# Kernel tuning notes

Measured on AMD Instinct MI355X. Metric: run time of the kernel, lower is better.

Reference implementation:

```python
import jax, jax.numpy as jnp
import numpy as np

B, S, IN, OUT, GS = 4, 2048, 4096, 16384, 32
G = IN // GS  # 128 groups per row


def setup_inputs() -> dict:
    key = jax.random.key(0)
    kx, ks, ki = jax.random.split(key, 3)
    x = jax.random.normal(kx, (B, S, IN), dtype=jnp.float32)
    # n_bits=2 initial codebook from the module
    codebook = jnp.array([-1.0, -0.25, 0.25, 1.0], dtype=jnp.float32)
    # scale is the log of per-group max-abs (use_exp_for_scale=True)
    scale = jax.random.normal(ks, (OUT, G, 1), dtype=jnp.float32) * 0.1 - 2.0
    indexes = jax.random.randint(ki, (OUT, G, GS), 0, 4, dtype=jnp.int32)
    return {"x": x, "codebook": codebook, "scale": scale, "indexes": indexes}


def reference(x, codebook, scale, indexes):
    # dequantize_weight: normalize codebook, gather per-element, exp-scale per group
    cb_norm = codebook / jnp.clip(jnp.max(jnp.abs(codebook)), 1e-8, None)
    w = cb_norm[indexes] * jnp.exp(scale)          # (OUT, G, GS)
    w = w.reshape(OUT, IN)                         # (OUT, IN)
    # F.linear(x, w) = x @ w.T
    return jnp.einsum("bsi,oi->bso", x, w)
```

## Files before the change

### kernel.cpp

```cpp
#include <hip/hip_runtime.h>
#include <stdint.h>


typedef unsigned short u16;
typedef __attribute__((ext_vector_type(8))) __bf16 bf16x8;
typedef __attribute__((ext_vector_type(4))) float f32x4;

__device__ __forceinline__ uint32_t f2bf(float f) {
  uint32_t u = __builtin_bit_cast(uint32_t, f);
  return (u + 0x7FFFu + ((u >> 16) & 1u)) >> 16;
}

__device__ __forceinline__ void gload16(const u16* g, u16* l) {
  __builtin_amdgcn_global_load_lds(
      (__attribute__((address_space(1))) void*)(g),
      (__attribute__((address_space(3))) void*)(l), 16, 0, 0);
}

__device__ __forceinline__ uint32_t sel4(uint32_t b0, uint32_t b1, uint32_t b2,
                                         uint32_t b3, int q) {
  uint32_t lo = (q & 1) ? b1 : b0;
  uint32_t hi = (q & 1) ? b3 : b2;
  return (q & 2) ? hi : lo;
}

__global__ __launch_bounds__(256) void cvt_x(const float* __restrict__ x,
                                             u16* __restrict__ xb, int n8) {
  int t = blockIdx.x * 256 + threadIdx.x;
  if (t >= n8) return;
  const float4* xp = reinterpret_cast<const float4*>(x) + (size_t)t * 2;
  float4 v0 = xp[0], v1 = xp[1];
  uint4 o;
  o.x = f2bf(v0.x) | (f2bf(v0.y) << 16);
  o.y = f2bf(v0.z) | (f2bf(v0.w) << 16);
  o.z = f2bf(v1.x) | (f2bf(v1.y) << 16);
  o.w = f2bf(v1.z) | (f2bf(v1.w) << 16);
  reinterpret_cast<uint4*>(xb)[t] = o;
}

__global__ __launch_bounds__(256) void dequant_w(
    const float* __restrict__ cb, const float* __restrict__ scale,
    const int* __restrict__ idx, u16* __restrict__ w, int ngroups) {
  int t = blockIdx.x * 256 + threadIdx.x;
  if (t >= ngroups) return;
  float m = fmaxf(fmaxf(fabsf(cb[0]), fabsf(cb[1])),
                  fmaxf(fabsf(cb[2]), fabsf(cb[3])));
  m = fmaxf(m, 1e-8f);
  float s = expf(scale[t]) / m;
  uint32_t b0 = f2bf(cb[0] * s), b1 = f2bf(cb[1] * s);
  uint32_t b2 = f2bf(cb[2] * s), b3 = f2bf(cb[3] * s);
  const int4* ip = reinterpret_cast<const int4*>(idx) + (size_t)t * 8;
  uint4* op = reinterpret_cast<uint4*>(w) + (size_t)t * 4;
#pragma unroll
  for (int v = 0; v < 4; ++v) {
    int4 qa = ip[v * 2], qb = ip[v * 2 + 1];
    uint4 o;
    o.x = sel4(b0, b1, b2, b3, qa.x) | (sel4(b0, b1, b2, b3, qa.y) << 16);
    o.y = sel4(b0, b1, b2, b3, qa.z) | (sel4(b0, b1, b2, b3, qa.w) << 16);
    o.z = sel4(b0, b1, b2, b3, qb.x) | (sel4(b0, b1, b2, b3, qb.y) << 16);
    o.w = sel4(b0, b1, b2, b3, qb.z) | (sel4(b0, b1, b2, b3, qb.w) << 16);
    op[v] = o;
  }
}

#define BM 256
#define BN 256
#define BK 64

__device__ __forceinline__ void memfence() { asm volatile("" ::: "memory"); }
__device__ __forceinline__ void BARx() {
  memfence();
  __builtin_amdgcn_s_barrier();
  memfence();
}

__global__ void __launch_bounds__(512, 2) gemm256(
    const u16* __restrict__ A, const u16* __restrict__ Bt,
    float* __restrict__ C, int M, int N, int K) {
  __shared__ u16 sm[2][2][BM * BK];

  const int nwg = gridDim.x;
  const int cpx = nwg >> 3;
  const int bid = blockIdx.x;
  const int swz = (bid & 7) * cpx + (bid >> 3);
  const int ntn = N / BN;
  const int m0 = (swz / ntn) * BM;
  const int n0 = (swz % ntn) * BN;

  const int tid = threadIdx.x;
  const int lane = tid & 63;
  const int wid = tid >> 6;
  const int wr = wid >> 2;
  const int wc = wid & 3;

  const int srow = wid * 8 + (lane >> 3);
  const int scol = (((lane & 7) ^ ((lane >> 3) & 7)) << 3);
  const u16* gA = A + (size_t)(m0 + srow) * K + scol;
  const u16* gB = Bt + (size_t)(n0 + srow) * K + scol;

#define STAGE(b, op, h, gp, kc)                                   \
  {                                                               \
    u16* d = &sm[(b)][(op)][(h)*8192 + wid * 512];                \
    const u16* g = (gp) + (size_t)((h)*128) * K + (kc);           \
    gload16(g, d);                                                \
    gload16(g + (size_t)64 * K, d + 4096);                        \
  }

  const int swzp0 = (((lane >> 4) ^ (lane & 7)) << 3);
  const int swzp1 = ((((lane >> 4) + 4) ^ (lane & 7)) << 3);
  const int lr = lane & 15;
  const int rAbase = (wr * 64 + lr) * BK;
  const int rBbase = (wc * 32 + lr) * BK;

  bf16x8 af[4][2], bv[2][2];

#define LOADA(b, q)                                               \
  {                                                               \
    const u16* p = &sm[(b)][0][rAbase + (q)*8192];                \
    af[0][0] = *(const bf16x8*)(p + swzp0);                       \
    af[0][1] = *(const bf16x8*)(p + swzp1);                       \
    af[1][0] = *(const bf16x8*)(p + 1024 + swzp0);                \
    af[1][1] = *(const bf16x8*)(p + 1024 + swzp1);                \
    af[2][0] = *(const bf16x8*)(p + 2048 + swzp0);                \
    af[2][1] = *(const bf16x8*)(p + 2048 + swzp1);                \
    af[3][0] = *(const bf16x8*)(p + 3072 + swzp0);                \
    af[3][1] = *(const bf16x8*)(p + 3072 + swzp1);                \
  }
#define LOADB(b, pp)                                              \
  {                                                               \
    const u16* p = &sm[(b)][1][rBbase + (pp)*8192];               \
    bv[0][0] = *(const bf16x8*)(p + swzp0);                       \
    bv[0][1] = *(const bf16x8*)(p + swzp1);                       \
    bv[1][0] = *(const bf16x8*)(p + 1024 + swzp0);                \
    bv[1][1] = *(const bf16x8*)(p + 1024 + swzp1);                \
  }
#define MFMAQ(q, pp)                                                        \
  {                                                                         \
    __builtin_amdgcn_s_setprio(1);                                          \
    _Pragma("unroll") for (int i = 0; i < 4; ++i)                           \
        _Pragma("unroll") for (int j = 0; j < 2; ++j)                       \
            _Pragma("unroll") for (int ks = 0; ks < 2; ++ks)                \
                acc[(q)*4 + i][(pp)*2 + j] =                                \
        __builtin_amdgcn_mfma_f32_16x16x32_bf16(                            \
            af[i][ks], bv[j][ks], acc[(q)*4 + i][(pp)*2 + j], 0, 0, 0);     \
    __builtin_amdgcn_s_setprio(0);                                          \
  }
#define VM6 asm volatile("s_waitcnt vmcnt(6)" ::: "memory");
#define VM0 asm volatile("s_waitcnt vmcnt(0)" ::: "memory");

  f32x4 acc[8][4];
#pragma unroll
  for (int i = 0; i < 8; ++i)
#pragma unroll
    for (int j = 0; j < 4; ++j) acc[i][j] = f32x4{0.f, 0.f, 0.f, 0.f};

  STAGE(0, 0, 0, gA, (size_t)0)
  STAGE(0, 1, 1, gB, (size_t)0)
  STAGE(0, 0, 1, gA, (size_t)0)
  STAGE(0, 1, 0, gB, (size_t)0)
  STAGE(1, 0, 0, gA, (size_t)64)
  STAGE(1, 1, 1, gB, (size_t)64)
  STAGE(1, 0, 1, gA, (size_t)64)
  VM6
  BARx();

#pragma unroll 1
  for (int i = 0; i < 31; ++i) {
    const size_t cS1 = (size_t)(2 * i + 1) * 64;
    const size_t cb0 = (size_t)(2 * i + 2) * 64;
    const size_t cb1 = (size_t)(2 * i + 3) * 64;
    LOADA(0, 0) LOADB(0, 0)
    STAGE(1, 1, 0, gB, cS1)
    BARx(); MFMAQ(0, 0) BARx();
    LOADB(0, 1)
    STAGE(0, 0, 0, gA, cb0)
    BARx(); MFMAQ(0, 1) BARx();
    LOADA(0, 1)
    STAGE(0, 1, 1, gB, cb0)
    BARx(); MFMAQ(1, 1) BARx();
    LOADB(0, 0)
    STAGE(0, 0, 1, gA, cb0)
    BARx(); MFMAQ(1, 0) VM6 BARx();
    LOADA(1, 0) LOADB(1, 0)
    STAGE(0, 1, 0, gB, cb0)
    BARx(); MFMAQ(0, 0) BARx();
    LOADB(1, 1)
    STAGE(1, 0, 0, gA, cb1)
    BARx(); MFMAQ(0, 1) BARx();
    LOADA(1, 1)
    STAGE(1, 1, 1, gB, cb1)
    BARx(); MFMAQ(1, 1) BARx();
    LOADB(1, 0)
    STAGE(1, 0, 1, gA, cb1)
    BARx(); MFMAQ(1, 0) VM6 BARx();
  }

  {
    const size_t cS1 = (size_t)63 * 64;
    LOADA(0, 0) LOADB(0, 0)
    STAGE(1, 1, 0, gB, cS1)
    BARx(); MFMAQ(0, 0) BARx();
    LOADB(0, 1)
    BARx(); MFMAQ(0, 1) BARx();
    LOADA(0, 1)
    BARx(); MFMAQ(1, 1) BARx();
    LOADB(0, 0)
    BARx(); MFMAQ(1, 0) VM0 BARx();
    LOADA(1, 0) LOADB(1, 0)
    BARx(); MFMAQ(0, 0) BARx();
    LOADB(1, 1)
    BARx(); MFMAQ(0, 1) BARx();
    LOADA(1, 1)
    BARx(); MFMAQ(1, 1) BARx();
    LOADB(1, 0)
    BARx(); MFMAQ(1, 0)
  }

  const int crow0 = m0 + wr * 64 + ((lane >> 4) << 2);
  const int ccol0 = n0 + wc * 32 + (lane & 15);
#pragma unroll
  for (int q = 0; q < 2; ++q)
#pragma unroll
    for (int mi = 0; mi < 4; ++mi)
#pragma unroll
      for (int r = 0; r < 4; ++r) {
        float* cp = C + (size_t)(crow0 + q * 128 + mi * 16 + r) * N + ccol0;
#pragma unroll
        for (int pp = 0; pp < 2; ++pp)
#pragma unroll
          for (int j = 0; j < 2; ++j)
            cp[pp * 128 + j * 16] = acc[q * 4 + mi][pp * 2 + j][r];
      }
}

extern "C" void kernel_launch(void* const* d_in, const int* in_sizes, int n_in,
                              void* d_out, int out_size, void* d_ws,
                              size_t ws_size, hipStream_t stream) {
  const float* x = (const float*)d_in[0];
  const float* cb = (const float*)d_in[1];
  const float* scale = (const float*)d_in[2];
  const int* idx = (const int*)d_in[3];
  float* out = (float*)d_out;

  constexpr int M = 4 * 2048;
  constexpr int N = 16384;
  constexpr int K = 4096;

  u16* xb = (u16*)d_ws;
  u16* wb = xb + (size_t)M * K;

  const int n8 = M * K / 8;
  cvt_x<<<dim3(n8 / 256), dim3(256), 0, stream>>>(x, xb, n8);
  const int ngroups = N * (K / 32);
  dequant_w<<<dim3(ngroups / 256), dim3(256), 0, stream>>>(cb, scale, idx, wb,
                                                           ngroups);
  gemm256<<<dim3((M / BM) * (N / BN)), dim3(512), 0, stream>>>(xb, wb, out, M,
                                                               N, K);
}
```

Baseline: 1.054 ms.

## Switch GEMM inner loop to 32x32x16 MFMA with batched LDS reads

Replaces the 16x16x32 bf16 MFMA tiling with 32x32x16 MFMAs, which changes the per-wave fragment layout, the LDS swizzled read offsets and the output store mapping. All A and B fragments for a K-half are now read from LDS once per buffer instead of being interleaved between MFMA quarters. The goal is fewer LDS reads per MFMA and higher MFMA throughput. In exchange the kernel holds more fragment registers at once, which may raise register pressure at 2 blocks per CU, and the LDS reads are no longer overlapped with the MFMA phases.

```diff
diff --git a/kernel.cpp b/kernel.cpp
--- a/kernel.cpp
+++ b/kernel.cpp
@@ -4,7 +4,7 @@
 
 typedef unsigned short u16;
 typedef __attribute__((ext_vector_type(8))) __bf16 bf16x8;
-typedef __attribute__((ext_vector_type(4))) float f32x4;
+typedef __attribute__((ext_vector_type(16))) float f32x16;
 
 __device__ __forceinline__ uint32_t f2bf(float f) {
   uint32_t u = __builtin_bit_cast(uint32_t, f);
@@ -90,8 +90,9 @@
   const int tid = threadIdx.x;
   const int lane = tid & 63;
   const int wid = tid >> 6;
-  const int wr = wid >> 2;
-  const int wc = wid & 3;
+  const int wr = wid >> 1;
+  const int wrm = wid >> 2;
+  const int wcn = wid & 3;
 
   const int srow = wid * 8 + (lane >> 3);
   const int scol = (((lane & 7) ^ ((lane >> 3) & 7)) << 3);
@@ -106,53 +107,53 @@
     gload16(g + (size_t)64 * K, d + 4096);                        \
   }
 
-  const int swzp0 = (((lane >> 4) ^ (lane & 7)) << 3);
-  const int swzp1 = ((((lane >> 4) + 4) ^ (lane & 7)) << 3);
-  const int lr = lane & 15;
-  const int rAbase = (wr * 64 + lr) * BK;
-  const int rBbase = (wc * 32 + lr) * BK;
-
-  bf16x8 af[4][2], bv[2][2];
-
-#define LOADA(b, q)                                               \
-  {                                                               \
-    const u16* p = &sm[(b)][0][rAbase + (q)*8192];                \
-    af[0][0] = *(const bf16x8*)(p + swzp0);                       \
-    af[0][1] = *(const bf16x8*)(p + swzp1);                       \
-    af[1][0] = *(const bf16x8*)(p + 1024 + swzp0);                \
-    af[1][1] = *(const bf16x8*)(p + 1024 + swzp1);                \
-    af[2][0] = *(const bf16x8*)(p + 2048 + swzp0);                \
-    af[2][1] = *(const bf16x8*)(p + 2048 + swzp1);                \
-    af[3][0] = *(const bf16x8*)(p + 3072 + swzp0);                \
-    af[3][1] = *(const bf16x8*)(p + 3072 + swzp1);                \
-  }
-#define LOADB(b, pp)                                              \
-  {                                                               \
-    const u16* p = &sm[(b)][1][rBbase + (pp)*8192];               \
-    bv[0][0] = *(const bf16x8*)(p + swzp0);                       \
-    bv[0][1] = *(const bf16x8*)(p + swzp1);                       \
-    bv[1][0] = *(const bf16x8*)(p + 1024 + swzp0);                \
-    bv[1][1] = *(const bf16x8*)(p + 1024 + swzp1);                \
-  }
-#define MFMAQ(q, pp)                                                        \
-  {                                                                         \
-    __builtin_amdgcn_s_setprio(1);                                          \
-    _Pragma("unroll") for (int i = 0; i < 4; ++i)                           \
-        _Pragma("unroll") for (int j = 0; j < 2; ++j)                       \
-            _Pragma("unroll") for (int ks = 0; ks < 2; ++ks)                \
-                acc[(q)*4 + i][(pp)*2 + j] =                                \
-        __builtin_amdgcn_mfma_f32_16x16x32_bf16(                            \
-            af[i][ks], bv[j][ks], acc[(q)*4 + i][(pp)*2 + j], 0, 0, 0);     \
-    __builtin_amdgcn_s_setprio(0);                                          \
+  const int l7 = lane & 7;
+  const int hi5 = lane >> 5;
+  const int l31 = lane & 31;
+  int sw[4];
+#pragma unroll
+  for (int ks = 0; ks < 4; ++ks) sw[ks] = (((ks * 2 + hi5) ^ l7) << 3);
+  const int rAoff = (wrm * 64 + l31) * BK;
+  const int rBoff = (wcn * 32 + l31) * BK;
+
+  bf16x8 a0[2][4], a1[2][4], bv[2][4];
+
+#define ALLREADS(b)                                                     \
+  {                                                                     \
+    const u16* pa = &sm[(b)][0][rAoff];                                 \
+    const u16* pb = &sm[(b)][1][rBoff];                                 \
+    _Pragma("unroll") for (int mi = 0; mi < 2; ++mi)                    \
+        _Pragma("unroll") for (int ks = 0; ks < 4; ++ks)                \
+            a0[mi][ks] = *(const bf16x8*)(pa + mi * 2048 + sw[ks]);     \
+    _Pragma("unroll") for (int ks = 0; ks < 4; ++ks)                    \
+        bv[0][ks] = *(const bf16x8*)(pb + sw[ks]);                      \
+    _Pragma("unroll") for (int ks = 0; ks < 4; ++ks)                    \
+        bv[1][ks] = *(const bf16x8*)(pb + 8192 + sw[ks]);               \
+    _Pragma("unroll") for (int mi = 0; mi < 2; ++mi)                    \
+        _Pragma("unroll") for (int ks = 0; ks < 4; ++ks)                \
+            a1[mi][ks] = *(const bf16x8*)(pa + 8192 + mi * 2048 + sw[ks]); \
+  }
+
+#define MFMAQ(q, pp, AF)                                                \
+  {                                                                     \
+    __builtin_amdgcn_s_setprio(1);                                      \
+    _Pragma("unroll") for (int mi = 0; mi < 2; ++mi)                    \
+        _Pragma("unroll") for (int ks = 0; ks < 4; ++ks)                \
+            acc[(q)*2 + mi][(pp)] =                                     \
+        __builtin_amdgcn_mfma_f32_32x32x16_bf16(                        \
+            AF[mi][ks], bv[(pp)][ks], acc[(q)*2 + mi][(pp)], 0, 0, 0);  \
+    __builtin_amdgcn_s_setprio(0);                                      \
   }
 #define VM6 asm volatile("s_waitcnt vmcnt(6)" ::: "memory");
 #define VM0 asm volatile("s_waitcnt vmcnt(0)" ::: "memory");
 
-  f32x4 acc[8][4];
-#pragma unroll
-  for (int i = 0; i < 8; ++i)
-#pragma unroll
-    for (int j = 0; j < 4; ++j) acc[i][j] = f32x4{0.f, 0.f, 0.f, 0.f};
+  f32x16 acc[4][2];
+#pragma unroll
+  for (int i = 0; i < 4; ++i)
+#pragma unroll
+    for (int j = 0; j < 2; ++j)
+#pragma unroll
+      for (int r = 0; r < 16; ++r) acc[i][j][r] = 0.f;
 
   STAGE(0, 0, 0, gA, (size_t)0)
   STAGE(0, 1, 1, gB, (size_t)0)
@@ -169,67 +170,53 @@
     const size_t cS1 = (size_t)(2 * i + 1) * 64;
     const size_t cb0 = (size_t)(2 * i + 2) * 64;
     const size_t cb1 = (size_t)(2 * i + 3) * 64;
-    LOADA(0, 0) LOADB(0, 0)
+    ALLREADS(0)
     STAGE(1, 1, 0, gB, cS1)
-    BARx(); MFMAQ(0, 0) BARx();
-    LOADB(0, 1)
+    BARx(); MFMAQ(0, 0, a0) BARx();
     STAGE(0, 0, 0, gA, cb0)
-    BARx(); MFMAQ(0, 1) BARx();
-    LOADA(0, 1)
+    BARx(); MFMAQ(0, 1, a0) BARx();
     STAGE(0, 1, 1, gB, cb0)
-    BARx(); MFMAQ(1, 1) BARx();
-    LOADB(0, 0)
+    BARx(); MFMAQ(1, 1, a1) BARx();
     STAGE(0, 0, 1, gA, cb0)
-    BARx(); MFMAQ(1, 0) VM6 BARx();
-    LOADA(1, 0) LOADB(1, 0)
+    BARx(); MFMAQ(1, 0, a1) VM6 BARx();
+    ALLREADS(1)
     STAGE(0, 1, 0, gB, cb0)
-    BARx(); MFMAQ(0, 0) BARx();
-    LOADB(1, 1)
+    BARx(); MFMAQ(0, 0, a0) BARx();
     STAGE(1, 0, 0, gA, cb1)
-    BARx(); MFMAQ(0, 1) BARx();
-    LOADA(1, 1)
+    BARx(); MFMAQ(0, 1, a0) BARx();
     STAGE(1, 1, 1, gB, cb1)
-    BARx(); MFMAQ(1, 1) BARx();
-    LOADB(1, 0)
+    BARx(); MFMAQ(1, 1, a1) BARx();
     STAGE(1, 0, 1, gA, cb1)
-    BARx(); MFMAQ(1, 0) VM6 BARx();
+    BARx(); MFMAQ(1, 0, a1) VM6 BARx();
   }
 
   {
     const size_t cS1 = (size_t)63 * 64;
-    LOADA(0, 0) LOADB(0, 0)
+    ALLREADS(0)
     STAGE(1, 1, 0, gB, cS1)
-    BARx(); MFMAQ(0, 0) BARx();
-    LOADB(0, 1)
-    BARx(); MFMAQ(0, 1) BARx();
-    LOADA(0, 1)
-    BARx(); MFMAQ(1, 1) BARx();
-    LOADB(0, 0)
-    BARx(); MFMAQ(1, 0) VM0 BARx();
-    LOADA(1, 0) LOADB(1, 0)
-    BARx(); MFMAQ(0, 0) BARx();
-    LOADB(1, 1)
-    BARx(); MFMAQ(0, 1) BARx();
-    LOADA(1, 1)
-    BARx(); MFMAQ(1, 1) BARx();
-    LOADB(1, 0)
-    BARx(); MFMAQ(1, 0)
-  }
-
-  const int crow0 = m0 + wr * 64 + ((lane >> 4) << 2);
-  const int ccol0 = n0 + wc * 32 + (lane & 15);
+    BARx(); MFMAQ(0, 0, a0) BARx();
+    BARx(); MFMAQ(0, 1, a0) BARx();
+    BARx(); MFMAQ(1, 1, a1) BARx();
+    BARx(); MFMAQ(1, 0, a1) VM0 BARx();
+    ALLREADS(1)
+    BARx(); MFMAQ(0, 0, a0) BARx();
+    BARx(); MFMAQ(0, 1, a0) BARx();
+    BARx(); MFMAQ(1, 1, a1) BARx();
+    MFMAQ(1, 0, a1)
+  }
+
+  const int crow = m0 + wrm * 64 + (hi5 << 2);
+  const int ccol = n0 + wcn * 32 + l31;
 #pragma unroll
   for (int q = 0; q < 2; ++q)
 #pragma unroll
-    for (int mi = 0; mi < 4; ++mi)
-#pragma unroll
-      for (int r = 0; r < 4; ++r) {
-        float* cp = C + (size_t)(crow0 + q * 128 + mi * 16 + r) * N + ccol0;
-#pragma unroll
-        for (int pp = 0; pp < 2; ++pp)
-#pragma unroll
-          for (int j = 0; j < 2; ++j)
-            cp[pp * 128 + j * 16] = acc[q * 4 + mi][pp * 2 + j][r];
+    for (int mi = 0; mi < 2; ++mi)
+#pragma unroll
+      for (int r = 0; r < 16; ++r) {
+        const int row = crow + q * 128 + mi * 32 + (r & 3) + ((r >> 2) << 3);
+        float* cp = C + (size_t)row * N + ccol;
+        cp[0] = acc[q * 2 + mi][0][r];
+        cp[128] = acc[q * 2 + mi][1][r];
       }
 }
 
```

Result: slower. 2.383 ms (+126.1%).

## Double-buffer B fragments in registers and halve barriers in GEMM main loop

Applied to the files above, without the earlier changes.

Splits the B register fragments into two sets (bv0/bv1) so the B tile for pp=0 stays live across the q-sweep and no longer has to be reloaded from LDS. This removes one LDS B reload per half-iteration and drops the trailing barrier after each MFMA quad, which cuts the number of workgroup barriers per step roughly in half. The global-to-LDS stage order is also reshuffled so the B halves are prefetched alongside A. The costs are extra VGPR pressure from the second fragment set and a tighter ordering argument for LDS reuse, since fewer barriers protect against buffer overwrite races.

```diff
diff --git a/kernel.cpp b/kernel.cpp
--- a/kernel.cpp
+++ b/kernel.cpp
@@ -112,7 +112,7 @@
   const int rAbase = (wr * 64 + lr) * BK;
   const int rBbase = (wc * 32 + lr) * BK;
 
-  bf16x8 af[4][2], bv[2][2];
+  bf16x8 af[4][2], bv0[2][2], bv1[2][2];
 
 #define LOADA(b, q)                                               \
   {                                                               \
@@ -126,15 +126,15 @@
     af[3][0] = *(const bf16x8*)(p + 3072 + swzp0);                \
     af[3][1] = *(const bf16x8*)(p + 3072 + swzp1);                \
   }
-#define LOADB(b, pp)                                              \
+#define LOADBX(BV, b, pp)                                         \
   {                                                               \
     const u16* p = &sm[(b)][1][rBbase + (pp)*8192];               \
-    bv[0][0] = *(const bf16x8*)(p + swzp0);                       \
-    bv[0][1] = *(const bf16x8*)(p + swzp1);                       \
-    bv[1][0] = *(const bf16x8*)(p + 1024 + swzp0);                \
-    bv[1][1] = *(const bf16x8*)(p + 1024 + swzp1);                \
-  }
-#define MFMAQ(q, pp)                                                        \
+    BV[0][0] = *(const bf16x8*)(p + swzp0);                       \
+    BV[0][1] = *(const bf16x8*)(p + swzp1);                       \
+    BV[1][0] = *(const bf16x8*)(p + 1024 + swzp0);                \
+    BV[1][1] = *(const bf16x8*)(p + 1024 + swzp1);                \
+  }
+#define MFMAQ(q, pp, BV)                                                    \
   {                                                                         \
     __builtin_amdgcn_s_setprio(1);                                          \
     _Pragma("unroll") for (int i = 0; i < 4; ++i)                           \
@@ -142,7 +142,7 @@
             _Pragma("unroll") for (int ks = 0; ks < 2; ++ks)                \
                 acc[(q)*4 + i][(pp)*2 + j] =                                \
         __builtin_amdgcn_mfma_f32_16x16x32_bf16(                            \
-            af[i][ks], bv[j][ks], acc[(q)*4 + i][(pp)*2 + j], 0, 0, 0);     \
+            af[i][ks], BV[j][ks], acc[(q)*4 + i][(pp)*2 + j], 0, 0, 0);     \
     __builtin_amdgcn_s_setprio(0);                                          \
   }
 #define VM6 asm volatile("s_waitcnt vmcnt(6)" ::: "memory");
@@ -155,65 +155,62 @@
     for (int j = 0; j < 4; ++j) acc[i][j] = f32x4{0.f, 0.f, 0.f, 0.f};
 
   STAGE(0, 0, 0, gA, (size_t)0)
+  STAGE(0, 1, 0, gB, (size_t)0)
   STAGE(0, 1, 1, gB, (size_t)0)
   STAGE(0, 0, 1, gA, (size_t)0)
-  STAGE(0, 1, 0, gB, (size_t)0)
   STAGE(1, 0, 0, gA, (size_t)64)
+  STAGE(1, 1, 0, gB, (size_t)64)
   STAGE(1, 1, 1, gB, (size_t)64)
-  STAGE(1, 0, 1, gA, (size_t)64)
   VM6
   BARx();
 
 #pragma unroll 1
   for (int i = 0; i < 31; ++i) {
-    const size_t cS1 = (size_t)(2 * i + 1) * 64;
-    const size_t cb0 = (size_t)(2 * i + 2) * 64;
-    const size_t cb1 = (size_t)(2 * i + 3) * 64;
-    LOADA(0, 0) LOADB(0, 0)
-    STAGE(1, 1, 0, gB, cS1)
-    BARx(); MFMAQ(0, 0) BARx();
-    LOADB(0, 1)
-    STAGE(0, 0, 0, gA, cb0)
-    BARx(); MFMAQ(0, 1) BARx();
+    const size_t cT1 = (size_t)(2 * i + 1) * 64;
+    const size_t cT2 = (size_t)(2 * i + 2) * 64;
+    const size_t cT3 = (size_t)(2 * i + 3) * 64;
+    LOADA(0, 0) LOADBX(bv0, 0, 0)
+    STAGE(1, 0, 1, gA, cT1)
+    BARx(); MFMAQ(0, 0, bv0)
+    LOADBX(bv1, 0, 1)
+    BARx(); MFMAQ(0, 1, bv1)
     LOADA(0, 1)
-    STAGE(0, 1, 1, gB, cb0)
-    BARx(); MFMAQ(1, 1) BARx();
-    LOADB(0, 0)
-    STAGE(0, 0, 1, gA, cb0)
-    BARx(); MFMAQ(1, 0) VM6 BARx();
-    LOADA(1, 0) LOADB(1, 0)
-    STAGE(0, 1, 0, gB, cb0)
-    BARx(); MFMAQ(0, 0) BARx();
-    LOADB(1, 1)
-    STAGE(1, 0, 0, gA, cb1)
-    BARx(); MFMAQ(0, 1) BARx();
+    STAGE(0, 0, 0, gA, cT2) STAGE(0, 1, 0, gB, cT2)
+    BARx(); MFMAQ(1, 1, bv1)
+    STAGE(0, 1, 1, gB, cT2)
+    VM6
+    BARx(); MFMAQ(1, 0, bv0)
+    LOADA(1, 0) LOADBX(bv0, 1, 0)
+    STAGE(0, 0, 1, gA, cT2)
+    BARx(); MFMAQ(0, 0, bv0)
+    LOADBX(bv1, 1, 1)
+    BARx(); MFMAQ(0, 1, bv1)
     LOADA(1, 1)
-    STAGE(1, 1, 1, gB, cb1)
-    BARx(); MFMAQ(1, 1) BARx();
-    LOADB(1, 0)
-    STAGE(1, 0, 1, gA, cb1)
-    BARx(); MFMAQ(1, 0) VM6 BARx();
+    STAGE(1, 0, 0, gA, cT3) STAGE(1, 1, 0, gB, cT3)
+    BARx(); MFMAQ(1, 1, bv1)
+    STAGE(1, 1, 1, gB, cT3)
+    VM6
+    BARx(); MFMAQ(1, 0, bv0)
   }
 
   {
-    const size_t cS1 = (size_t)63 * 64;
-    LOADA(0, 0) LOADB(0, 0)
-    STAGE(1, 1, 0, gB, cS1)
-    BARx(); MFMAQ(0, 0) BARx();
-    LOADB(0, 1)
-    BARx(); MFMAQ(0, 1) BARx();
+    const size_t cT1 = (size_t)63 * 64;
+    LOADA(0, 0) LOADBX(bv0, 0, 0)
+    STAGE(1, 0, 1, gA, cT1)
+    BARx(); MFMAQ(0, 0, bv0)
+    LOADBX(bv1, 0, 1)
+    BARx(); MFMAQ(0, 1, bv1)
     LOADA(0, 1)
-    BARx(); MFMAQ(1, 1) BARx();
-    LOADB(0, 0)
-    BARx(); MFMAQ(1, 0) VM0 BARx();
-    LOADA(1, 0) LOADB(1, 0)
-    BARx(); MFMAQ(0, 0) BARx();
-    LOADB(1, 1)
-    BARx(); MFMAQ(0, 1) BARx();
+    BARx(); MFMAQ(1, 1, bv1)
+    VM0
+    BARx(); MFMAQ(1, 0, bv0)
+    LOADA(1, 0) LOADBX(bv0, 1, 0)
+    BARx(); MFMAQ(0, 0, bv0)
+    LOADBX(bv1, 1, 1)
+    BARx(); MFMAQ(0, 1, bv1)
     LOADA(1, 1)
-    BARx(); MFMAQ(1, 1) BARx();
-    LOADB(1, 0)
-    BARx(); MFMAQ(1, 0)
+    BARx(); MFMAQ(1, 1, bv1)
+    BARx(); MFMAQ(1, 0, bv0)
   }
 
   const int crow0 = m0 + wr * 64 + ((lane >> 4) << 2);
```

Measured after the change: 1.027 ms. 1.03x faster.
